# Kernel optimization log

Measured on AMD Instinct MI355X. Metric: run time of the kernel, lower is better.

Reference implementation:

```python
import jax, jax.numpy as jnp
import numpy as np

N = 100000      # user + item nodes
E = 600000      # number of edges
LATDIM = 128
HEAD = 4
HDIM = LATDIM // HEAD


def setup_inputs() -> dict:
    key = jax.random.key(0)
    ks = jax.random.split(key, 7)
    return {
        "embeds": jax.random.normal(ks[0], (N, LATDIM), dtype=jnp.float32),
        "qTrans": jax.random.normal(ks[1], (LATDIM, LATDIM), dtype=jnp.float32) * (1.0 / np.sqrt(LATDIM)),
        "kTrans": jax.random.normal(ks[2], (LATDIM, LATDIM), dtype=jnp.float32) * (1.0 / np.sqrt(LATDIM)),
        "vTrans": jax.random.normal(ks[3], (LATDIM, LATDIM), dtype=jnp.float32) * (1.0 / np.sqrt(LATDIM)),
        "filt": jax.random.normal(ks[4], (N, HEAD), dtype=jnp.float32),
        "rows": jax.random.randint(ks[5], (E,), 0, N, dtype=jnp.int32),
        "cols": jax.random.randint(ks[6], (E,), 0, N, dtype=jnp.int32),
    }


def reference(embeds, qTrans, kTrans, vTrans, filt, rows, cols):
    # gather endpoint embeddings: [E, latdim]
    rowEmbeds = embeds[rows]
    colEmbeds = embeds[cols]
    # per-edge multi-head q/k/v: [E, H, D]
    qEmbeds = (rowEmbeds @ qTrans).reshape(E, HEAD, HDIM)
    kEmbeds = (colEmbeds @ kTrans).reshape(E, HEAD, HDIM)
    vEmbeds = (colEmbeds @ vTrans).reshape(E, HEAD, HDIM)
    # per-edge per-head attention logits
    att = jnp.einsum('ehd,ehd->eh', qEmbeds, kEmbeds)
    att = jnp.clip(att, -10.0, 10.0)
    att = att + filt[cols]
    expAtt = jnp.exp(att)
    # segment softmax over destination rows
    attNorm = jax.ops.segment_sum(expAtt, rows, num_segments=N)[rows]
    att = expAtt / (attNorm + 1e-8)
    # weighted values, scatter-sum back to nodes
    resEdges = (att[:, :, None] * vEmbeds).reshape(E, LATDIM)
    resEmbeds = jax.ops.segment_sum(resEdges, rows, num_segments=N)
    return resEmbeds
```

## Files before the change

### kernel.cpp

```cpp
#include <hip/hip_runtime.h>

#define N_NODES 100000
#define E_EDGES 600000
#define LATDIM 128
#define HEAD 4
#define HDIM 32

#define SCAN_NB 98

typedef _Float16 f16x8 __attribute__((ext_vector_type(8)));
typedef _Float16 f16x2 __attribute__((ext_vector_type(2)));
typedef float    f32x4 __attribute__((ext_vector_type(4)));

__device__ __forceinline__ unsigned f32_to_bf16_rne(float x) {
    unsigned u = __float_as_uint(x);
    u += 0x7fffu + ((u >> 16) & 1u);
    return u >> 16;
}

__device__ __forceinline__ float dot4_f16(unsigned k01, unsigned k23,
                                          unsigned q01, unsigned q23) {
#if defined(__has_builtin)
#if __has_builtin(__builtin_amdgcn_fdot2)
    float r = __builtin_amdgcn_fdot2(__builtin_bit_cast(f16x2, k01),
                                     __builtin_bit_cast(f16x2, q01), 0.f, false);
    return  __builtin_amdgcn_fdot2(__builtin_bit_cast(f16x2, k23),
                                   __builtin_bit_cast(f16x2, q23), r, false);
#else
    f16x2 a = __builtin_bit_cast(f16x2, k01), b = __builtin_bit_cast(f16x2, q01);
    f16x2 c = __builtin_bit_cast(f16x2, k23), d = __builtin_bit_cast(f16x2, q23);
    return (float)a[0]*(float)b[0] + (float)a[1]*(float)b[1]
         + (float)c[0]*(float)d[0] + (float)c[1]*(float)d[1];
#endif
#else
    f16x2 a = __builtin_bit_cast(f16x2, k01), b = __builtin_bit_cast(f16x2, q01);
    f16x2 c = __builtin_bit_cast(f16x2, k23), d = __builtin_bit_cast(f16x2, q23);
    return (float)a[0]*(float)b[0] + (float)a[1]*(float)b[1]
         + (float)c[0]*(float)d[0] + (float)c[1]*(float)d[1];
#endif
}

__global__ __launch_bounds__(256) void wprep_kernel(
    const float* __restrict__ qT, const float* __restrict__ kT,
    const float* __restrict__ vT,
    unsigned short* __restrict__ WT,
    int* __restrict__ counts, unsigned* __restrict__ state)
{
    int g = blockIdx.x * 256 + threadIdx.x;

    for (int i = g; i < N_NODES; i += SCAN_NB * 256) counts[i] = 0;
    if (g < 128) state[g] = 0u;

    if (g >= 3072) return;
    int m    = g >> 10;
    int rem  = g & 1023;
    int c    = rem >> 3;
    int k0   = (rem & 7) * 16;
    const float* W = (m == 0) ? qT : (m == 1) ? kT : vT;

    unsigned short hv[16];
    #pragma unroll
    for (int j = 0; j < 16; ++j) {
        _Float16 h = (_Float16)W[(size_t)(k0 + j) * 128 + c];
        hv[j] = __builtin_bit_cast(unsigned short, h);
    }
    size_t off = (size_t)m * 16384 + (size_t)c * 128 + k0;
    *(uint4*)(WT + off)     = *(const uint4*)&hv[0];
    *(uint4*)(WT + off + 8) = *(const uint4*)&hv[8];
}

__global__ __launch_bounds__(256) void qkv_mfma_kernel(
    const float* __restrict__ embeds,
    const unsigned short* __restrict__ WT,
    const int* __restrict__ rows,
    int* __restrict__ counts,
    unsigned short* __restrict__ Qh, unsigned* __restrict__ KV)
{
    __shared__ __align__(16) char smem[32768];
    char* R0 = smem;
    char* R1 = smem + 16384;

    const int tid = threadIdx.x;
    const int rowBase = blockIdx.x * 64;

    uint4 pb0, pb1, pb2, pb3;

#define PF(MN, HN) do {                                                          \
        const char* _s = (const char*)(WT + (size_t)(MN) * 16384                 \
                                          + (size_t)(HN) * 8192);                \
        pb0 = *(const uint4*)(_s + (size_t)(0 * 256 + tid) * 16);                \
        pb1 = *(const uint4*)(_s + (size_t)(1 * 256 + tid) * 16);                \
        pb2 = *(const uint4*)(_s + (size_t)(2 * 256 + tid) * 16);                \
        pb3 = *(const uint4*)(_s + (size_t)(3 * 256 + tid) * 16);                \
    } while (0)

#define COMMIT(R) do {                                                           \
        { int _i = 0 * 256 + tid; int _c = _i >> 4;                              \
          int _s = (_c * 256 + (_i & 15) * 16) ^ ((_c & 7) << 4);                \
          *(uint4*)((R) + _s) = pb0; }                                           \
        { int _i = 1 * 256 + tid; int _c = _i >> 4;                              \
          int _s = (_c * 256 + (_i & 15) * 16) ^ ((_c & 7) << 4);                \
          *(uint4*)((R) + _s) = pb1; }                                           \
        { int _i = 2 * 256 + tid; int _c = _i >> 4;                              \
          int _s = (_c * 256 + (_i & 15) * 16) ^ ((_c & 7) << 4);                \
          *(uint4*)((R) + _s) = pb2; }                                           \
        { int _i = 3 * 256 + tid; int _c = _i >> 4;                              \
          int _s = (_c * 256 + (_i & 15) * 16) ^ ((_c & 7) << 4);                \
          *(uint4*)((R) + _s) = pb3; }                                           \
    } while (0)

#define MFMA_M(ACC, R) do {                                                      \
        _Pragma("unroll")                                                        \
        for (int kk = 0; kk < 4; ++kk) {                                         \
            _Pragma("unroll")                                                    \
            for (int n = 0; n < 4; ++n) {                                        \
                int col  = n * 16 + lrow;                                        \
                int byte = (col * 256 + kk * 64 + kg * 16) ^ ((lrow & 7) << 4);  \
                f16x8 b = __builtin_bit_cast(f16x8, *(const uint4*)((R) + byte)); \
                ACC[n] = __builtin_amdgcn_mfma_f32_16x16x32_f16(a[kk], b, ACC[n], 0, 0, 0); \
            }                                                                    \
        }                                                                        \
    } while (0)

#define ZACC(ACC) f32x4 ACC[4] = { {0.f,0.f,0.f,0.f}, {0.f,0.f,0.f,0.f},         \
                                   {0.f,0.f,0.f,0.f}, {0.f,0.f,0.f,0.f} }

#define STORE_Q(ACC, H) do {                                                     \
        _Pragma("unroll")                                                        \
        for (int n = 0; n < 4; ++n)                                              \
        _Pragma("unroll")                                                        \
        for (int j = 0; j < 4; ++j) {                                            \
            int gr  = rowBase + wv * 16 + kg * 4 + j;                            \
            int col = (H) * 64 + n * 16 + lrow;                                  \
            if (gr < N_NODES)                                                    \
                Qh[(size_t)gr * 128 + col] =                                     \
                    __builtin_bit_cast(unsigned short, (_Float16)ACC[n][j]);     \
        }                                                                        \
    } while (0)

#define STORE_KV(ACC, H) do {                                                    \
        _Pragma("unroll")                                                        \
        for (int n = 0; n < 4; ++n)                                              \
        _Pragma("unroll")                                                        \
        for (int j = 0; j < 4; ++j) {                                            \
            int gr  = rowBase + wv * 16 + kg * 4 + j;                            \
            int col = (H) * 64 + n * 16 + lrow;                                  \
            if (gr < N_NODES) {                                                  \
                unsigned pk = (unsigned)__builtin_bit_cast(unsigned short,       \
                                  (_Float16)kreg[n][j])                          \
                            | (f32_to_bf16_rne(ACC[n][j]) << 16);                \
                KV[(size_t)gr * 128 + col] = pk;                                 \
            }                                                                    \
        }                                                                        \
    } while (0)

    PF(0, 0);

    #pragma unroll
    for (int it = 0; it < 4; ++it) {
        int idx = it * 256 + tid;
        int r   = idx >> 4;
        int c16 = idx & 15;
        int gr  = rowBase + r;
        float4 u0 = make_float4(0.f, 0.f, 0.f, 0.f), u1 = u0;
        if (gr < N_NODES) {
            const float* p = embeds + (size_t)gr * 128 + c16 * 8;
            u0 = *(const float4*)p;
            u1 = *(const float4*)(p + 4);
        }
        f16x8 v;
        v[0] = (_Float16)u0.x; v[1] = (_Float16)u0.y;
        v[2] = (_Float16)u0.z; v[3] = (_Float16)u0.w;
        v[4] = (_Float16)u1.x; v[5] = (_Float16)u1.y;
        v[6] = (_Float16)u1.z; v[7] = (_Float16)u1.w;
        int byte = (r * 256 + c16 * 16) ^ ((r & 7) << 4);
        *(uint4*)(R0 + byte) = __builtin_bit_cast(uint4, v);
    }
    __syncthreads();

    const int lane = tid & 63;
    const int wv   = tid >> 6;
    const int lrow = lane & 15;
    const int kg   = lane >> 4;

    f16x8 a[4];
    {
        const int arow = wv * 16 + lrow;
        #pragma unroll
        for (int kk = 0; kk < 4; ++kk) {
            int byte = (arow * 256 + kk * 64 + kg * 16) ^ ((lrow & 7) << 4);
            a[kk] = __builtin_bit_cast(f16x8, *(const uint4*)(R0 + byte));
        }
    }
    COMMIT(R1);
    __syncthreads();

    f32x4 kreg[4];

    {
        PF(1, 0); ZACC(acc);
        MFMA_M(acc, R1);
        STORE_Q(acc, 0);
        COMMIT(R0); __syncthreads();
    }
    {
        PF(2, 0); ZACC(acc);
        MFMA_M(acc, R0);
        kreg[0] = acc[0]; kreg[1] = acc[1]; kreg[2] = acc[2]; kreg[3] = acc[3];
        COMMIT(R1); __syncthreads();
    }
    {
        PF(0, 1); ZACC(acc);
        MFMA_M(acc, R1);
        STORE_KV(acc, 0);
        COMMIT(R0); __syncthreads();
    }
    {
        PF(1, 1); ZACC(acc);
        MFMA_M(acc, R0);
        STORE_Q(acc, 1);
        COMMIT(R1); __syncthreads();
    }
    {
        PF(2, 1); ZACC(acc);
        MFMA_M(acc, R1);
        kreg[0] = acc[0]; kreg[1] = acc[1]; kreg[2] = acc[2]; kreg[3] = acc[3];
        COMMIT(R0); __syncthreads();
    }
    {
        ZACC(acc);
        MFMA_M(acc, R0);
        STORE_KV(acc, 1);
    }

    for (int e = blockIdx.x * 256 + tid; e < E_EDGES; e += gridDim.x * 256)
        atomicAdd(&counts[rows[e]], 1);

#undef PF
#undef COMMIT
#undef MFMA_M
#undef ZACC
#undef STORE_Q
#undef STORE_KV
}

__global__ __launch_bounds__(256) void scan_lb_kernel(
    const int* __restrict__ counts, int* __restrict__ starts,
    int* __restrict__ cursor, unsigned* __restrict__ state)
{
    __shared__ int s[256];
    __shared__ int bcast;
    int b = blockIdx.x, t = threadIdx.x;
    int base = b * 1024 + t * 4;
    int v0 = (base + 0 < N_NODES) ? counts[base + 0] : 0;
    int v1 = (base + 1 < N_NODES) ? counts[base + 1] : 0;
    int v2 = (base + 2 < N_NODES) ? counts[base + 2] : 0;
    int v3 = (base + 3 < N_NODES) ? counts[base + 3] : 0;
    int local = v0 + v1 + v2 + v3;
    s[t] = local;
    __syncthreads();
    for (int off = 1; off < 256; off <<= 1) {
        int x = (t >= off) ? s[t - off] : 0;
        __syncthreads();
        s[t] += x;
        __syncthreads();
    }
    int incl  = s[t];
    int excl  = incl - local;
    int total = s[255];

    if (t == 0) {
        if (b == 0) {
            atomicExch(&state[0], ((unsigned)total << 2) | 2u);
            bcast = 0;
        } else {
            atomicExch(&state[b], ((unsigned)total << 2) | 1u);
        }
    }

    if (b > 0 && t < 64) {
        int sum  = 0;
        int wbase = b - 1;
        while (true) {
            int idx = wbase - t;
            unsigned w = (idx >= 0)
                       ? atomicAdd(&state[idx], 0u)
                       : 2u;
            unsigned st = w & 3u;
            unsigned long long m0 = __ballot(st == 0u);
            unsigned long long m2 = __ballot(st == 2u);
            int p = m2 ? (int)(__ffsll((unsigned long long)m2) - 1) : 64;
            unsigned long long below =
                (p < 64) ? ((1ull << p) - 1ull) : ~0ull;
            bool clean = ((m0 & below) == 0ull) && (p < 64 ? true : m0 == 0ull);
            if (clean) {
                int contrib = (t <= p) ? (int)(w >> 2) : 0;
                contrib += __shfl_down(contrib, 32);
                contrib += __shfl_down(contrib, 16);
                contrib += __shfl_down(contrib, 8);
                contrib += __shfl_down(contrib, 4);
                contrib += __shfl_down(contrib, 2);
                contrib += __shfl_down(contrib, 1);
                if (t == 0) sum += contrib;
                if (p < 64) break;
                wbase -= 64;
            }
        }
        if (t == 0) {
            atomicExch(&state[b], ((unsigned)(sum + total) << 2) | 2u);
            bcast = sum;
        }
    }
    __syncthreads();
    int e = excl + bcast;
    if (base + 0 < N_NODES) { starts[base + 0] = e;                cursor[base + 0] = e; }
    if (base + 1 < N_NODES) { starts[base + 1] = e + v0;           cursor[base + 1] = e + v0; }
    if (base + 2 < N_NODES) { starts[base + 2] = e + v0 + v1;      cursor[base + 2] = e + v0 + v1; }
    if (base + 3 < N_NODES) { starts[base + 3] = e + v0 + v1 + v2; cursor[base + 3] = e + v0 + v1 + v2; }
}

__global__ __launch_bounds__(256) void scatter_kernel(
    const int* __restrict__ rows, const int* __restrict__ cols,
    int* __restrict__ cursor, int* __restrict__ csrCols)
{
    int e = blockIdx.x * 256 + threadIdx.x;
    if (e >= E_EDGES) return;
    int pos = atomicAdd(&cursor[rows[e]], 1);
    csrCols[pos] = cols[e];
}

__global__ __launch_bounds__(256) void att_agg_kernel(
    const unsigned short* __restrict__ Qh, const unsigned* __restrict__ KV,
    const float* __restrict__ filt,
    const int* __restrict__ starts, const int* __restrict__ counts,
    const int* __restrict__ csrCols,
    float* __restrict__ out)
{
    int t = threadIdx.x;
    int node = blockIdx.x * 8 + (t >> 5);
    if (node >= N_NODES) return;
    int lane = t & 31;
    int h = lane >> 3;

    uint2 qp = *(const uint2*)(Qh + (size_t)node * 128 + lane * 4);
    int s    = starts[node];
    int cnt  = counts[node];
    int last = cnt - 1;

    float norm = 0.f;
    float ax = 0.f, ay = 0.f, az = 0.f, aw = 0.f;

    int   a_c0, a_c1, a_c2, a_c3,  b_c0, b_c1, b_c2, b_c3;
    float a_f0, a_f1, a_f2, a_f3,  b_f0, b_f1, b_f2, b_f3;
    uint4 a_k0, a_k1, a_k2, a_k3,  b_k0, b_k1, b_k2, b_k3;

#define LOADB(P, I) do {                                                        \
        int _i1 = (I) + 1 < last ? (I) + 1 : last;                              \
        int _i2 = (I) + 2 < last ? (I) + 2 : last;                              \
        int _i3 = (I) + 3 < last ? (I) + 3 : last;                              \
        P##_c0 = csrCols[s + (I)];  P##_c1 = csrCols[s + _i1];                  \
        P##_c2 = csrCols[s + _i2];  P##_c3 = csrCols[s + _i3];                  \
        P##_k0 = ((const uint4*)KV)[(size_t)P##_c0 * 32 + lane];                \
        P##_k1 = ((const uint4*)KV)[(size_t)P##_c1 * 32 + lane];                \
        P##_k2 = ((const uint4*)KV)[(size_t)P##_c2 * 32 + lane];                \
        P##_k3 = ((const uint4*)KV)[(size_t)P##_c3 * 32 + lane];                \
        P##_f0 = filt[P##_c0 * HEAD + h];  P##_f1 = filt[P##_c1 * HEAD + h];    \
        P##_f2 = filt[P##_c2 * HEAD + h];  P##_f3 = filt[P##_c3 * HEAD + h];    \
    } while (0)

#define EDGE(KVU, F, VALID) {                                                   \
        unsigned k01 = ((KVU).x & 0xffffu) | ((KVU).y << 16);                   \
        unsigned k23 = ((KVU).z & 0xffffu) | ((KVU).w << 16);                   \
        float p = dot4_f16(k01, k23, qp.x, qp.y);                               \
        float v0f = __uint_as_float((KVU).x & 0xffff0000u);                     \
        float v1f = __uint_as_float((KVU).y & 0xffff0000u);                     \
        float v2f = __uint_as_float((KVU).z & 0xffff0000u);                     \
        float v3f = __uint_as_float((KVU).w & 0xffff0000u);                     \
        p += __shfl_xor(p, 1);                                                  \
        p += __shfl_xor(p, 2);                                                  \
        p += __shfl_xor(p, 4);                                                  \
        float w = __expf(fminf(fmaxf(p, -10.f), 10.f) + (F));                   \
        w = (VALID) ? w : 0.f;                                                  \
        norm += w;                                                              \
        ax += w * v0f; ay += w * v1f; az += w * v2f; aw += w * v3f; }

#define CONSUME(P, I) do {                                                      \
        bool _m1 = (I) + 1 <= last;                                             \
        bool _m2 = (I) + 2 <= last;                                             \
        bool _m3 = (I) + 3 <= last;                                             \
        EDGE(P##_k0, P##_f0, true);                                             \
        EDGE(P##_k1, P##_f1, _m1);                                              \
        EDGE(P##_k2, P##_f2, _m2);                                              \
        EDGE(P##_k3, P##_f3, _m3);                                              \
    } while (0)

    if (cnt > 0) {
        LOADB(a, 0);
        int i = 0;
        while (true) {
            if (i + 4 < cnt) LOADB(b, i + 4);
            CONSUME(a, i);
            i += 4;
            if (i >= cnt) break;
            if (i + 4 < cnt) LOADB(a, i + 4);
            CONSUME(b, i);
            i += 4;
            if (i >= cnt) break;
        }
    }
#undef LOADB
#undef EDGE
#undef CONSUME

    float inv = 1.0f / (norm + 1e-8f);
    ((float4*)(out + (size_t)node * 128))[lane] =
        make_float4(ax * inv, ay * inv, az * inv, aw * inv);
}

extern "C" void kernel_launch(void* const* d_in, const int* in_sizes, int n_in,
                              void* d_out, int out_size, void* d_ws, size_t ws_size,
                              hipStream_t stream) {
    const float* embeds = (const float*)d_in[0];
    const float* qT     = (const float*)d_in[1];
    const float* kT     = (const float*)d_in[2];
    const float* vT     = (const float*)d_in[3];
    const float* filt   = (const float*)d_in[4];
    const int*   rows   = (const int*)d_in[5];
    const int*   cols   = (const int*)d_in[6];
    float*       out    = (float*)d_out;

    unsigned short* Qh = (unsigned short*)d_ws;
    unsigned* KV   = (unsigned*)(Qh + (size_t)N_NODES * 128);
    int* counts    = (int*)(KV + (size_t)N_NODES * 128);
    int* starts    = counts + N_NODES;
    int* cursor    = starts + N_NODES;
    int* csrCols   = cursor + N_NODES;
    unsigned* state = (unsigned*)(csrCols + E_EDGES);

    unsigned short* WT = (unsigned short*)csrCols;

    wprep_kernel<<<SCAN_NB, 256, 0, stream>>>(qT, kT, vT, WT, counts, state);
    qkv_mfma_kernel<<<(N_NODES + 63) / 64, 256, 0, stream>>>(
        embeds, WT, rows, counts, Qh, KV);
    scan_lb_kernel<<<SCAN_NB, 256, 0, stream>>>(counts, starts, cursor, state);
    scatter_kernel<<<(E_EDGES + 255) / 256, 256, 0, stream>>>(rows, cols, cursor, csrCols);
    att_agg_kernel<<<(N_NODES + 7) / 8, 256, 0, stream>>>(
        Qh, KV, filt, starts, counts, csrCols, out);
}
```

Measured before the change: 240.7 us.

## Drop LDS staging in QKV projection; load weight fragments directly from global

Result: slower. 296.3 us (+23.1%).

```diff
diff --git a/kernel.cpp b/kernel.cpp
--- a/kernel.cpp
+++ b/kernel.cpp
@@ -76,95 +76,21 @@
     int* __restrict__ counts,
     unsigned short* __restrict__ Qh, unsigned* __restrict__ KV)
 {
-    __shared__ __align__(16) char smem[32768];
-    char* R0 = smem;
-    char* R1 = smem + 16384;
-
-    const int tid = threadIdx.x;
-    const int rowBase = blockIdx.x * 64;
-
-    uint4 pb0, pb1, pb2, pb3;
-
-#define PF(MN, HN) do {                                                          \
-        const char* _s = (const char*)(WT + (size_t)(MN) * 16384                 \
-                                          + (size_t)(HN) * 8192);                \
-        pb0 = *(const uint4*)(_s + (size_t)(0 * 256 + tid) * 16);                \
-        pb1 = *(const uint4*)(_s + (size_t)(1 * 256 + tid) * 16);                \
-        pb2 = *(const uint4*)(_s + (size_t)(2 * 256 + tid) * 16);                \
-        pb3 = *(const uint4*)(_s + (size_t)(3 * 256 + tid) * 16);                \
-    } while (0)
-
-#define COMMIT(R) do {                                                           \
-        { int _i = 0 * 256 + tid; int _c = _i >> 4;                              \
-          int _s = (_c * 256 + (_i & 15) * 16) ^ ((_c & 7) << 4);                \
-          *(uint4*)((R) + _s) = pb0; }                                           \
-        { int _i = 1 * 256 + tid; int _c = _i >> 4;                              \
-          int _s = (_c * 256 + (_i & 15) * 16) ^ ((_c & 7) << 4);                \
-          *(uint4*)((R) + _s) = pb1; }                                           \
-        { int _i = 2 * 256 + tid; int _c = _i >> 4;                              \
-          int _s = (_c * 256 + (_i & 15) * 16) ^ ((_c & 7) << 4);                \
-          *(uint4*)((R) + _s) = pb2; }                                           \
-        { int _i = 3 * 256 + tid; int _c = _i >> 4;                              \
-          int _s = (_c * 256 + (_i & 15) * 16) ^ ((_c & 7) << 4);                \
-          *(uint4*)((R) + _s) = pb3; }                                           \
-    } while (0)
-
-#define MFMA_M(ACC, R) do {                                                      \
-        _Pragma("unroll")                                                        \
-        for (int kk = 0; kk < 4; ++kk) {                                         \
-            _Pragma("unroll")                                                    \
-            for (int n = 0; n < 4; ++n) {                                        \
-                int col  = n * 16 + lrow;                                        \
-                int byte = (col * 256 + kk * 64 + kg * 16) ^ ((lrow & 7) << 4);  \
-                f16x8 b = __builtin_bit_cast(f16x8, *(const uint4*)((R) + byte)); \
-                ACC[n] = __builtin_amdgcn_mfma_f32_16x16x32_f16(a[kk], b, ACC[n], 0, 0, 0); \
-            }                                                                    \
-        }                                                                        \
-    } while (0)
-
-#define ZACC(ACC) f32x4 ACC[4] = { {0.f,0.f,0.f,0.f}, {0.f,0.f,0.f,0.f},         \
-                                   {0.f,0.f,0.f,0.f}, {0.f,0.f,0.f,0.f} }
-
-#define STORE_Q(ACC, H) do {                                                     \
-        _Pragma("unroll")                                                        \
-        for (int n = 0; n < 4; ++n)                                              \
-        _Pragma("unroll")                                                        \
-        for (int j = 0; j < 4; ++j) {                                            \
-            int gr  = rowBase + wv * 16 + kg * 4 + j;                            \
-            int col = (H) * 64 + n * 16 + lrow;                                  \
-            if (gr < N_NODES)                                                    \
-                Qh[(size_t)gr * 128 + col] =                                     \
-                    __builtin_bit_cast(unsigned short, (_Float16)ACC[n][j]);     \
-        }                                                                        \
-    } while (0)
-
-#define STORE_KV(ACC, H) do {                                                    \
-        _Pragma("unroll")                                                        \
-        for (int n = 0; n < 4; ++n)                                              \
-        _Pragma("unroll")                                                        \
-        for (int j = 0; j < 4; ++j) {                                            \
-            int gr  = rowBase + wv * 16 + kg * 4 + j;                            \
-            int col = (H) * 64 + n * 16 + lrow;                                  \
-            if (gr < N_NODES) {                                                  \
-                unsigned pk = (unsigned)__builtin_bit_cast(unsigned short,       \
-                                  (_Float16)kreg[n][j])                          \
-                            | (f32_to_bf16_rne(ACC[n][j]) << 16);                \
-                KV[(size_t)gr * 128 + col] = pk;                                 \
-            }                                                                    \
-        }                                                                        \
-    } while (0)
-
-    PF(0, 0);
-
+    const int tid  = threadIdx.x;
+    const int lane = tid & 63;
+    const int wv   = tid >> 6;
+    const int lrow = lane & 15;
+    const int kg   = lane >> 4;
+    const int rowT = blockIdx.x * 64 + wv * 16;
+    const int arow = rowT + lrow;
+    const bool rok = arow < N_NODES;
+
+    f16x8 a[4];
     #pragma unroll
-    for (int it = 0; it < 4; ++it) {
-        int idx = it * 256 + tid;
-        int r   = idx >> 4;
-        int c16 = idx & 15;
-        int gr  = rowBase + r;
+    for (int kk = 0; kk < 4; ++kk) {
         float4 u0 = make_float4(0.f, 0.f, 0.f, 0.f), u1 = u0;
-        if (gr < N_NODES) {
-            const float* p = embeds + (size_t)gr * 128 + c16 * 8;
+        if (rok) {
+            const float* p = embeds + (size_t)arow * 128 + kk * 32 + kg * 8;
             u0 = *(const float4*)p;
             u1 = *(const float4*)(p + 4);
         }
@@ -173,75 +99,51 @@
         v[2] = (_Float16)u0.z; v[3] = (_Float16)u0.w;
         v[4] = (_Float16)u1.x; v[5] = (_Float16)u1.y;
         v[6] = (_Float16)u1.z; v[7] = (_Float16)u1.w;
-        int byte = (r * 256 + c16 * 16) ^ ((r & 7) << 4);
-        *(uint4*)(R0 + byte) = __builtin_bit_cast(uint4, v);
-    }
-    __syncthreads();
-
-    const int lane = tid & 63;
-    const int wv   = tid >> 6;
-    const int lrow = lane & 15;
-    const int kg   = lane >> 4;
-
-    f16x8 a[4];
-    {
-        const int arow = wv * 16 + lrow;
+        a[kk] = v;
+    }
+
+    const int orow = rowT + kg * 4;
+
+    #pragma unroll 2
+    for (int ct = 0; ct < 8; ++ct) {
+        const int col = ct * 16 + lrow;
+        const unsigned short* Wb = WT + (size_t)col * 128 + kg * 8;
+
+        f32x4 accq = {0.f, 0.f, 0.f, 0.f};
         #pragma unroll
         for (int kk = 0; kk < 4; ++kk) {
-            int byte = (arow * 256 + kk * 64 + kg * 16) ^ ((lrow & 7) << 4);
-            a[kk] = __builtin_bit_cast(f16x8, *(const uint4*)(R0 + byte));
-        }
-    }
-    COMMIT(R1);
-    __syncthreads();
-
-    f32x4 kreg[4];
-
-    {
-        PF(1, 0); ZACC(acc);
-        MFMA_M(acc, R1);
-        STORE_Q(acc, 0);
-        COMMIT(R0); __syncthreads();
-    }
-    {
-        PF(2, 0); ZACC(acc);
-        MFMA_M(acc, R0);
-        kreg[0] = acc[0]; kreg[1] = acc[1]; kreg[2] = acc[2]; kreg[3] = acc[3];
-        COMMIT(R1); __syncthreads();
-    }
-    {
-        PF(0, 1); ZACC(acc);
-        MFMA_M(acc, R1);
-        STORE_KV(acc, 0);
-        COMMIT(R0); __syncthreads();
-    }
-    {
-        PF(1, 1); ZACC(acc);
-        MFMA_M(acc, R0);
-        STORE_Q(acc, 1);
-        COMMIT(R1); __syncthreads();
-    }
-    {
-        PF(2, 1); ZACC(acc);
-        MFMA_M(acc, R1);
-        kreg[0] = acc[0]; kreg[1] = acc[1]; kreg[2] = acc[2]; kreg[3] = acc[3];
-        COMMIT(R0); __syncthreads();
-    }
-    {
-        ZACC(acc);
-        MFMA_M(acc, R0);
-        STORE_KV(acc, 1);
+            f16x8 b = *(const f16x8*)(Wb + kk * 32);
+            accq = __builtin_amdgcn_mfma_f32_16x16x32_f16(a[kk], b, accq, 0, 0, 0);
+        }
+        f32x4 acck = {0.f, 0.f, 0.f, 0.f};
+        #pragma unroll
+        for (int kk = 0; kk < 4; ++kk) {
+            f16x8 b = *(const f16x8*)(Wb + 16384 + kk * 32);
+            acck = __builtin_amdgcn_mfma_f32_16x16x32_f16(a[kk], b, acck, 0, 0, 0);
+        }
+        f32x4 accv = {0.f, 0.f, 0.f, 0.f};
+        #pragma unroll
+        for (int kk = 0; kk < 4; ++kk) {
+            f16x8 b = *(const f16x8*)(Wb + 32768 + kk * 32);
+            accv = __builtin_amdgcn_mfma_f32_16x16x32_f16(a[kk], b, accv, 0, 0, 0);
+        }
+
+        #pragma unroll
+        for (int j = 0; j < 4; ++j) {
+            int gr = orow + j;
+            if (gr < N_NODES) {
+                Qh[(size_t)gr * 128 + col] =
+                    __builtin_bit_cast(unsigned short, (_Float16)accq[j]);
+                unsigned pk = (unsigned)__builtin_bit_cast(unsigned short,
+                                  (_Float16)acck[j])
+                            | (f32_to_bf16_rne(accv[j]) << 16);
+                KV[(size_t)gr * 128 + col] = pk;
+            }
+        }
     }
 
     for (int e = blockIdx.x * 256 + tid; e < E_EDGES; e += gridDim.x * 256)
         atomicAdd(&counts[rows[e]], 1);
-
-#undef PF
-#undef COMMIT
-#undef MFMA_M
-#undef ZACC
-#undef STORE_Q
-#undef STORE_KV
 }
 
 __global__ __launch_bounds__(256) void scan_lb_kernel(
```
